# Optimization experiments

Measured on AMD Instinct MI355X. Metric: run time of the kernel, lower is better.

## Reference

```python
import jax, jax.numpy as jnp
import numpy as np

B, T, D, H = 8, 2048, 1024, 128  # batch, seq (== block_size), n_embd, head_size


def setup_inputs() -> dict:
    key = jax.random.key(0)
    kx, kq, kk, kv = jax.random.split(key, 4)
    s = D ** -0.5  # rough linear-init scale
    return {
        "x": jax.random.normal(kx, (B, T, D), dtype=jnp.float32),
        "Wq": jax.random.normal(kq, (D, H), dtype=jnp.float32) * s,
        "Wk": jax.random.normal(kk, (D, H), dtype=jnp.float32) * s,
        "Wv": jax.random.normal(kv, (D, H), dtype=jnp.float32) * s,
    }


def reference(x, Wq, Wk, Wv):
    # Linear projections (no bias)
    q = x @ Wq  # [B, T, H]
    k = x @ Wk  # [B, T, H]
    v = x @ Wv  # [B, T, H]
    scale = k.shape[-1] ** -0.5
    scores = jnp.einsum("bth,bsh->bts", q, k) * scale  # [B, T, T]
    # causal mask from tril buffer
    causal = jnp.tril(jnp.ones((T, T), dtype=bool))
    scores = jnp.where(causal, scores, jnp.finfo(scores.dtype).min)
    att = jax.nn.softmax(scores, axis=-1)
    out = jnp.einsum("bts,bsh->bth", att, v)  # [B, T, H]
    return out
```

## Files before the change

### kernel.cpp

```cpp
#include <hip/hip_runtime.h>
#include <hip/hip_bf16.h>
#include <stdint.h>

typedef float f32x4 __attribute__((ext_vector_type(4)));
typedef __bf16 bf16x8 __attribute__((ext_vector_type(8)));

#define T_SEQ 2048
#define D_EMB 1024
#define H_DIM 128
#define NBATCH 8
#define NTOK 16384

typedef __attribute__((address_space(3))) uint32_t lds_u32;
typedef const __attribute__((address_space(1))) uint32_t glb_u32;

#define DPPF(x, ctrl)                                                    \
  __int_as_float(__builtin_amdgcn_update_dpp(                            \
      0, __float_as_int(x), (ctrl), 0xF, 0xF, true))

#define PIPE_FENCE()                                       \
  do {                                                     \
    asm volatile("s_waitcnt vmcnt(0)" ::: "memory");       \
    __builtin_amdgcn_s_barrier();                          \
    __builtin_amdgcn_sched_barrier(0);                     \
  } while (0)


__global__ __launch_bounds__(256) void prep_w_kernel(
    const float* __restrict__ Wq, const float* __restrict__ Wk,
    const float* __restrict__ Wv, __hip_bfloat16* __restrict__ Wt) {
  __shared__ float T[128][133];
  const int mat = blockIdx.x >> 3;
  const int kc = blockIdx.x & 7;
  const float* W = (mat == 0) ? Wq : ((mat == 1) ? Wk : Wv);
  const int tid = threadIdx.x;
  const int k0 = kc * 128;
#pragma unroll 8
  for (int i = 0; i < 64; ++i) {
    const int e = i * 256 + tid;
    const int k = e >> 7, h = e & 127;
    T[k][h] = W[(size_t)(k0 + k) * H_DIM + h];
  }
  __syncthreads();
#pragma unroll 8
  for (int i = 0; i < 64; ++i) {
    const int e = i * 256 + tid;
    const int h = e >> 7, k = e & 127;
    Wt[((size_t)mat * 128 + h) * D_EMB + k0 + k] = __float2bfloat16(T[k][h]);
  }
}

__global__ __launch_bounds__(512) void proj_kernel(
    const float* __restrict__ x, const __hip_bfloat16* __restrict__ Wt,
    __hip_bfloat16* __restrict__ qb, __hip_bfloat16* __restrict__ kb,
    __hip_bfloat16* __restrict__ vt) {
  __shared__ __align__(16) float Af[2][64 * 64];
  __shared__ __align__(16) __hip_bfloat16 Bs[2][384 * 64];
  const int tid = threadIdx.x;
  const int wave = tid >> 6;
  const int lane = tid & 63;
  const int g = lane >> 4;
  const int lr = lane & 15;
  const int m0 = blockIdx.x * 64;
  const int wc = wave * 48;

  f32x4 acc[4][3];
#pragma unroll
  for (int m = 0; m < 4; ++m)
#pragma unroll
    for (int n = 0; n < 3; ++n) acc[m][n] = f32x4{0.f, 0.f, 0.f, 0.f};

  auto stageA = [&](int buf, int k0) {
#pragma unroll
    for (int i = 0; i < 2; ++i) {
      const int e = i * 512 + tid;
      const int row = e >> 4;
      const int un = e & 15;
      __builtin_amdgcn_global_load_lds(
          (glb_u32*)(uintptr_t)(x + (size_t)(m0 + row) * D_EMB + k0 +
                                ((un ^ (row & 15)) * 4)),
          (lds_u32*)(uintptr_t)(&Af[buf][e * 4]), 16, 0, 0);
    }
  };
  auto stageB = [&](int buf, int k0) {
#pragma unroll
    for (int i = 0; i < 6; ++i) {
      const int u = i * 512 + tid;
      const int row = u >> 3;
      const int chunk = u & 7;
      __builtin_amdgcn_global_load_lds(
          (glb_u32*)(uintptr_t)(Wt + (size_t)row * D_EMB + k0 +
                                ((chunk ^ (row & 7)) * 8)),
          (lds_u32*)(uintptr_t)(&Bs[buf][row * 64 + chunk * 8]), 16, 0, 0);
    }
  };
  auto compute = [&](int buf) {
#pragma unroll
    for (int kk = 0; kk < 2; ++kk) {
      bf16x8 a[4];
#pragma unroll
      for (int m = 0; m < 4; ++m) {
        const int row = m * 16 + lr;
        const int u0 = kk * 8 + g * 2;
        const f32x4 lo = *reinterpret_cast<const f32x4*>(
            &Af[buf][row * 64 + ((u0 ^ (row & 15)) * 4)]);
        const f32x4 hi = *reinterpret_cast<const f32x4*>(
            &Af[buf][row * 64 + (((u0 + 1) ^ (row & 15)) * 4)]);
        union { bf16x8 v; __hip_bfloat16 h[8]; } u;
        u.h[0] = __float2bfloat16(lo[0]);
        u.h[1] = __float2bfloat16(lo[1]);
        u.h[2] = __float2bfloat16(lo[2]);
        u.h[3] = __float2bfloat16(lo[3]);
        u.h[4] = __float2bfloat16(hi[0]);
        u.h[5] = __float2bfloat16(hi[1]);
        u.h[6] = __float2bfloat16(hi[2]);
        u.h[7] = __float2bfloat16(hi[3]);
        a[m] = u.v;
      }
#pragma unroll
      for (int n = 0; n < 3; ++n) {
        const int row = wc + n * 16 + lr;
        bf16x8 b = *reinterpret_cast<const bf16x8*>(
            &Bs[buf][row * 64 + (((kk * 4 + g) ^ (row & 7)) * 8)]);
#pragma unroll
        for (int m = 0; m < 4; ++m)
          acc[m][n] =
              __builtin_amdgcn_mfma_f32_16x16x32_bf16(a[m], b, acc[m][n], 0, 0, 0);
      }
    }
  };

  stageA(0, 0);
  stageB(0, 0);

  int cur = 0;
  for (int k = 0; k < 16; ++k) {
    PIPE_FENCE();
    if (k < 15) {
      stageA(cur ^ 1, (k + 1) * 64);
      stageB(cur ^ 1, (k + 1) * 64);
    }
    compute(cur);
    cur ^= 1;
  }

#pragma unroll
  for (int n = 0; n < 3; ++n) {
    const int ng = wc + n * 16 + lr;
    const int head = ng >> 7;
    const int h = ng & 127;
#pragma unroll
    for (int m = 0; m < 4; ++m) {
#pragma unroll
      for (int r = 0; r < 4; ++r) {
        const int row = m0 + m * 16 + g * 4 + r;
        const __hip_bfloat16 val = __float2bfloat16(acc[m][n][r]);
        if (head == 0) {
          qb[(size_t)row * H_DIM + h] = val;
        } else if (head == 1) {
          kb[(size_t)row * H_DIM + h] = val;
        } else {
          const int bi = row >> 11;
          const int t = row & (T_SEQ - 1);
          vt[((size_t)bi * H_DIM + h) * T_SEQ + t] = val;
        }
      }
    }
  }
}

__global__ __launch_bounds__(512) void attn_kernel(
    const __hip_bfloat16* __restrict__ qb, const __hip_bfloat16* __restrict__ kb,
    const __hip_bfloat16* __restrict__ vt, float* __restrict__ out,
    float* __restrict__ PA_O, float* __restrict__ PA_ml,
    float* __restrict__ PB_O, float* __restrict__ PB_ml) {
  __shared__ __align__(16) __hip_bfloat16 KV[2][16384];
  __shared__ __align__(16) __hip_bfloat16 Pl[8][16][40];
  __shared__ float Obuf[4][16][132];
  __shared__ float mbuf[8][16];
  __shared__ float lbuf[8][16];

  const int tid = threadIdx.x;
  const int wave = tid >> 6;
  const int lane = tid & 63;
  const int g = lane >> 4;
  const int lr = lane & 15;
  const int qt = wave >> 1;
  const int kp = wave & 1;
  const int idx = blockIdx.x;
  const int b = idx & 7;
  const int u = idx >> 3;

  const __hip_bfloat16* qB = qb + (size_t)b * T_SEQ * H_DIM;
  const __hip_bfloat16* kB = kb + (size_t)b * T_SEQ * H_DIM;
  const __hip_bfloat16* vB = vt + (size_t)b * H_DIM * T_SEQ;
  const float scale = 0.08838834764831845f;

  auto stage = [&](__hip_bfloat16* buf, int s0) {
#pragma unroll
    for (int i = 0; i < 2; ++i) {
      const int uu = tid + i * 512;
      const int row = uu >> 4, grp = uu & 15;
      __builtin_amdgcn_global_load_lds(
          (glb_u32*)(uintptr_t)(kB + (size_t)(s0 + row) * H_DIM +
                                ((grp ^ (row & 15)) * 8)),
          (lds_u32*)(uintptr_t)(buf + uu * 8), 16, 0, 0);
    }
#pragma unroll
    for (int i = 0; i < 2; ++i) {
      const int uu = tid + i * 512;
      const int h = uu >> 3, grp = uu & 7;
      __builtin_amdgcn_global_load_lds(
          (glb_u32*)(uintptr_t)(vB + (size_t)h * T_SEQ + s0 +
                                ((grp ^ (h & 7)) * 8)),
          (lds_u32*)(uintptr_t)(buf + 8192 + uu * 8), 16, 0, 0);
    }
  };

  auto process = [&](int tile, int rr0, int rr1, int mode) {
    const int qrow0 = tile * 64 + qt * 16;
    bf16x8 qf[4];
#pragma unroll
    for (int kt = 0; kt < 4; ++kt)
      qf[kt] = *reinterpret_cast<const bf16x8*>(
          qB + (size_t)(qrow0 + lr) * H_DIM + kt * 32 + g * 8);

    f32x4 oacc[8];
#pragma unroll
    for (int i = 0; i < 8; ++i) oacc[i] = f32x4{0.f, 0.f, 0.f, 0.f};
    float mrow[4] = {-1e30f, -1e30f, -1e30f, -1e30f};
    float lrow[4] = {0.f, 0.f, 0.f, 0.f};

    __hip_bfloat16* bufA = &KV[0][0];
    __hip_bfloat16* bufB = &KV[1][0];
    stage(bufA, rr0 * 64);

    for (int r = rr0; r <= rr1; ++r) {
      PIPE_FENCE();
      if (r < rr1) stage(bufB, (r + 1) * 64);
      const int s0 = r * 64;
      const bool active = (s0 + kp * 32) <= (qrow0 + 15);
      if (active) {
        f32x4 sacc[2];
        sacc[0] = f32x4{0.f, 0.f, 0.f, 0.f};
        sacc[1] = f32x4{0.f, 0.f, 0.f, 0.f};
#pragma unroll
        for (int nt = 0; nt < 2; ++nt) {
          const int kl = kp * 32 + nt * 16 + lr;
          const __hip_bfloat16* kr = bufA + kl * 128;
#pragma unroll
          for (int kt = 0; kt < 4; ++kt) {
            bf16x8 kf = *reinterpret_cast<const bf16x8*>(
                kr + (((kt * 4 + g) ^ (kl & 15)) * 8));
            sacc[nt] = __builtin_amdgcn_mfma_f32_16x16x32_bf16(qf[kt], kf,
                                                               sacc[nt], 0, 0, 0);
          }
        }
        bf16x8 vf[8];
#pragma unroll
        for (int ht = 0; ht < 8; ++ht) {
          const int h = ht * 16 + lr;
          vf[ht] = *reinterpret_cast<const bf16x8*>(
              bufA + 8192 + h * 64 + (((kp * 4 + g) ^ (h & 7)) * 8));
        }
        float sv[2][4];
#pragma unroll
        for (int nt = 0; nt < 2; ++nt)
#pragma unroll
          for (int rr = 0; rr < 4; ++rr) {
            const int key = s0 + kp * 32 + nt * 16 + lr;
            const int qr = qrow0 + g * 4 + rr;
            const float s = sacc[nt][rr] * scale;
            sv[nt][rr] = (key > qr) ? -1e30f : s;
          }
        float pm[4];
#pragma unroll
        for (int rr = 0; rr < 4; ++rr) pm[rr] = fmaxf(sv[0][rr], sv[1][rr]);
#pragma unroll
        for (int rr = 0; rr < 4; ++rr) {
          pm[rr] = fmaxf(pm[rr], DPPF(pm[rr], 0xB1));
          pm[rr] = fmaxf(pm[rr], DPPF(pm[rr], 0x4E));
          pm[rr] = fmaxf(pm[rr], DPPF(pm[rr], 0x141));
          pm[rr] = fmaxf(pm[rr], DPPF(pm[rr], 0x140));
        }
        bool ok = true;
#pragma unroll
        for (int rr = 0; rr < 4; ++rr) ok = ok && (pm[rr] <= mrow[rr] + 8.f);
        if (!__all((int)ok)) {
#pragma unroll
          for (int rr = 0; rr < 4; ++rr) {
            const float mnew = fmaxf(mrow[rr], pm[rr]);
            const float corr = __expf(mrow[rr] - mnew);
            mrow[rr] = mnew;
            lrow[rr] *= corr;
#pragma unroll
            for (int ht = 0; ht < 8; ++ht) oacc[ht][rr] *= corr;
          }
        }
        float rs[4];
#pragma unroll
        for (int rr = 0; rr < 4; ++rr) {
          const float p0 = __expf(sv[0][rr] - mrow[rr]);
          const float p1 = __expf(sv[1][rr] - mrow[rr]);
          Pl[wave][g * 4 + rr][lr] = __float2bfloat16(p0);
          Pl[wave][g * 4 + rr][16 + lr] = __float2bfloat16(p1);
          rs[rr] = p0 + p1;
        }
#pragma unroll
        for (int rr = 0; rr < 4; ++rr) {
          rs[rr] += DPPF(rs[rr], 0xB1);
          rs[rr] += DPPF(rs[rr], 0x4E);
          rs[rr] += DPPF(rs[rr], 0x141);
          rs[rr] += DPPF(rs[rr], 0x140);
        }
#pragma unroll
        for (int rr = 0; rr < 4; ++rr) lrow[rr] += rs[rr];
        bf16x8 pf = *reinterpret_cast<const bf16x8*>(&Pl[wave][lr][g * 8]);
#pragma unroll
        for (int ht = 0; ht < 8; ++ht)
          oacc[ht] = __builtin_amdgcn_mfma_f32_16x16x32_bf16(pf, vf[ht],
                                                             oacc[ht], 0, 0, 0);
      }
      __hip_bfloat16* t = bufA; bufA = bufB; bufB = t;
    }

    __syncthreads();
    if (kp == 1) {
#pragma unroll
      for (int ht = 0; ht < 8; ++ht)
#pragma unroll
        for (int rr = 0; rr < 4; ++rr)
          Obuf[qt][g * 4 + rr][ht * 16 + lr] = oacc[ht][rr];
      if (lr == 0) {
#pragma unroll
        for (int rr = 0; rr < 4; ++rr) {
          mbuf[wave][g * 4 + rr] = mrow[rr];
          lbuf[wave][g * 4 + rr] = lrow[rr];
        }
      }
    }
    __syncthreads();
    if (kp == 0) {
#pragma unroll
      for (int rr = 0; rr < 4; ++rr) {
        const float mB = mbuf[wave + 1][g * 4 + rr];
        const float lB = lbuf[wave + 1][g * 4 + rr];
        const float M = fmaxf(mrow[rr], mB);
        const float a = __expf(mrow[rr] - M);
        const float bt = __expf(mB - M);
        lrow[rr] = a * lrow[rr] + bt * lB;
        mrow[rr] = M;
#pragma unroll
        for (int ht = 0; ht < 8; ++ht)
          oacc[ht][rr] =
              a * oacc[ht][rr] + bt * Obuf[qt][g * 4 + rr][ht * 16 + lr];
      }
      if (mode == 0) {
#pragma unroll
        for (int ht = 0; ht < 8; ++ht)
#pragma unroll
          for (int rr = 0; rr < 4; ++rr) {
            const int qr = qrow0 + g * 4 + rr;
            out[((size_t)b * T_SEQ + qr) * H_DIM + ht * 16 + lr] =
                oacc[ht][rr] / lrow[rr];
          }
      } else {
        float* PO = (mode == 1) ? PA_O : PB_O;
        float* Pm = (mode == 1) ? PA_ml : PB_ml;
        const int slot = tile - 16;
#pragma unroll
        for (int rr = 0; rr < 4; ++rr) {
          const size_t pr = (size_t)(b * 16 + slot) * 64 + qt * 16 + g * 4 + rr;
#pragma unroll
          for (int ht = 0; ht < 8; ++ht)
            PO[pr * 128 + ht * 16 + lr] = oacc[ht][rr];
          if (lr == 0) {
            Pm[pr * 2 + 0] = mrow[rr];
            Pm[pr * 2 + 1] = lrow[rr];
          }
        }
      }
    }
    __syncthreads();
  };

  if (u < 16) {
    process(u, 0, u, 0);
    process(31 - u, 0, 15 - u, 1);
  } else {
    const int v = u - 16;
    process(31 - v, 16 - v, 31 - v, 2);
  }
}

__global__ __launch_bounds__(256) void combine_kernel(
    const float* __restrict__ PA_O, const float* __restrict__ PA_ml,
    const float* __restrict__ PB_O, const float* __restrict__ PB_ml,
    float* __restrict__ out) {
  const int b = blockIdx.x >> 4;
  const int s = blockIdx.x & 15;
  const int tid = threadIdx.x;
  const int row = tid >> 2;
  const int c0 = (tid & 3) * 32;
  const size_t pr = (size_t)(b * 16 + s) * 64 + row;
  const float mA = PA_ml[pr * 2], lA = PA_ml[pr * 2 + 1];
  const float mB = PB_ml[pr * 2], lB = PB_ml[pr * 2 + 1];
  const float M = fmaxf(mA, mB);
  const float a = __expf(mA - M), bb = __expf(mB - M);
  const float inv = 1.f / (a * lA + bb * lB);
  const float* oa = PA_O + pr * 128 + c0;
  const float* ob = PB_O + pr * 128 + c0;
  float* op = out + ((size_t)b * T_SEQ + (16 + s) * 64 + row) * H_DIM + c0;
#pragma unroll
  for (int i = 0; i < 32; i += 4) {
    const float4 x = *reinterpret_cast<const float4*>(oa + i);
    const float4 y = *reinterpret_cast<const float4*>(ob + i);
    float4 z;
    z.x = (a * x.x + bb * y.x) * inv;
    z.y = (a * x.y + bb * y.y) * inv;
    z.z = (a * x.z + bb * y.z) * inv;
    z.w = (a * x.w + bb * y.w) * inv;
    *reinterpret_cast<float4*>(op + i) = z;
  }
}

extern "C" void kernel_launch(void* const* d_in, const int* in_sizes, int n_in,
                              void* d_out, int out_size, void* d_ws, size_t ws_size,
                              hipStream_t stream) {
  const float* x = (const float*)d_in[0];
  const float* Wq = (const float*)d_in[1];
  const float* Wk = (const float*)d_in[2];
  const float* Wv = (const float*)d_in[3];
  float* out = (float*)d_out;

  __hip_bfloat16* Wt = (__hip_bfloat16*)d_ws;
  __hip_bfloat16* qbuf = Wt + (size_t)3 * 128 * 1024;
  __hip_bfloat16* kbuf = qbuf + (size_t)NTOK * H_DIM;
  __hip_bfloat16* vbuf = kbuf + (size_t)NTOK * H_DIM;
  float* fbase = (float*)(vbuf + (size_t)NBATCH * H_DIM * T_SEQ);
  float* PA_O = fbase;
  float* PA_ml = PA_O + (size_t)1048576;
  float* PB_O = PA_ml + 16384;
  float* PB_ml = PB_O + (size_t)1048576;

  hipLaunchKernelGGL(prep_w_kernel, dim3(24), dim3(256), 0, stream, Wq, Wk, Wv, Wt);
  hipLaunchKernelGGL(proj_kernel, dim3(256), dim3(512), 0, stream, x, Wt, qbuf,
                     kbuf, vbuf);
  hipLaunchKernelGGL(attn_kernel, dim3(256), dim3(512), 0, stream, qbuf, kbuf,
                     vbuf, out, PA_O, PA_ml, PB_O, PB_ml);
  hipLaunchKernelGGL(combine_kernel, dim3(128), dim3(256), 0, stream, PA_O,
                     PA_ml, PB_O, PB_ml, out);
}
```

Measured before the change: 70.64 us.

## Replace direct global-to-LDS loads with register-staged prefetch in proj and attention

Both the projection GEMM and the attention kernel drop the global_load_lds direct-to-LDS path. Next-tile data is now loaded into registers before compute and written to LDS afterwards, with a plain __syncthreads replacing the vmcnt(0)+barrier fence. In the projection kernel, x is converted to bf16 once at LDS-write time instead of in every compute read, which halves A-tile LDS space and bandwidth. The cost is extra VGPRs to hold the prefetched tiles and an added LDS write pass per iteration.

```diff
diff --git a/kernel.cpp b/kernel.cpp
--- a/kernel.cpp
+++ b/kernel.cpp
@@ -11,19 +11,9 @@
 #define NBATCH 8
 #define NTOK 16384
 
-typedef __attribute__((address_space(3))) uint32_t lds_u32;
-typedef const __attribute__((address_space(1))) uint32_t glb_u32;
-
 #define DPPF(x, ctrl)                                                    \
   __int_as_float(__builtin_amdgcn_update_dpp(                            \
       0, __float_as_int(x), (ctrl), 0xF, 0xF, true))
-
-#define PIPE_FENCE()                                       \
-  do {                                                     \
-    asm volatile("s_waitcnt vmcnt(0)" ::: "memory");       \
-    __builtin_amdgcn_s_barrier();                          \
-    __builtin_amdgcn_sched_barrier(0);                     \
-  } while (0)
 
 
 __global__ __launch_bounds__(256) void prep_w_kernel(
@@ -54,7 +44,7 @@
     const float* __restrict__ x, const __hip_bfloat16* __restrict__ Wt,
     __hip_bfloat16* __restrict__ qb, __hip_bfloat16* __restrict__ kb,
     __hip_bfloat16* __restrict__ vt) {
-  __shared__ __align__(16) float Af[2][64 * 64];
+  __shared__ __align__(16) __hip_bfloat16 As[2][64 * 64];
   __shared__ __align__(16) __hip_bfloat16 Bs[2][384 * 64];
   const int tid = threadIdx.x;
   const int wave = tid >> 6;
@@ -70,28 +60,44 @@
 #pragma unroll
     for (int n = 0; n < 3; ++n) acc[m][n] = f32x4{0.f, 0.f, 0.f, 0.f};
 
-  auto stageA = [&](int buf, int k0) {
-#pragma unroll
-    for (int i = 0; i < 2; ++i) {
-      const int e = i * 512 + tid;
-      const int row = e >> 4;
-      const int un = e & 15;
-      __builtin_amdgcn_global_load_lds(
-          (glb_u32*)(uintptr_t)(x + (size_t)(m0 + row) * D_EMB + k0 +
-                                ((un ^ (row & 15)) * 4)),
-          (lds_u32*)(uintptr_t)(&Af[buf][e * 4]), 16, 0, 0);
-    }
-  };
-  auto stageB = [&](int buf, int k0) {
+  const int arow = tid >> 3;
+  const int achunk = tid & 7;
+  const float* asrc = x + (size_t)(m0 + arow) * D_EMB + achunk * 8;
+
+  float4 fa0, fa1;
+  bf16x8 fb[6];
+
+  auto loads = [&](int k0) {
+    fa0 = *reinterpret_cast<const float4*>(asrc + k0);
+    fa1 = *reinterpret_cast<const float4*>(asrc + k0 + 4);
 #pragma unroll
     for (int i = 0; i < 6; ++i) {
       const int u = i * 512 + tid;
       const int row = u >> 3;
       const int chunk = u & 7;
-      __builtin_amdgcn_global_load_lds(
-          (glb_u32*)(uintptr_t)(Wt + (size_t)row * D_EMB + k0 +
-                                ((chunk ^ (row & 7)) * 8)),
-          (lds_u32*)(uintptr_t)(&Bs[buf][row * 64 + chunk * 8]), 16, 0, 0);
+      fb[i] = *reinterpret_cast<const bf16x8*>(
+          Wt + (size_t)row * D_EMB + k0 + chunk * 8);
+    }
+  };
+  auto writes = [&](int buf) {
+    union { bf16x8 v; __hip_bfloat16 h[8]; } u;
+    u.h[0] = __float2bfloat16(fa0.x);
+    u.h[1] = __float2bfloat16(fa0.y);
+    u.h[2] = __float2bfloat16(fa0.z);
+    u.h[3] = __float2bfloat16(fa0.w);
+    u.h[4] = __float2bfloat16(fa1.x);
+    u.h[5] = __float2bfloat16(fa1.y);
+    u.h[6] = __float2bfloat16(fa1.z);
+    u.h[7] = __float2bfloat16(fa1.w);
+    *reinterpret_cast<bf16x8*>(
+        &As[buf][arow * 64 + ((achunk ^ (arow & 7)) * 8)]) = u.v;
+#pragma unroll
+    for (int i = 0; i < 6; ++i) {
+      const int uu = i * 512 + tid;
+      const int row = uu >> 3;
+      const int chunk = uu & 7;
+      *reinterpret_cast<bf16x8*>(
+          &Bs[buf][row * 64 + ((chunk ^ (row & 7)) * 8)]) = fb[i];
     }
   };
   auto compute = [&](int buf) {
@@ -101,27 +107,14 @@
 #pragma unroll
       for (int m = 0; m < 4; ++m) {
         const int row = m * 16 + lr;
-        const int u0 = kk * 8 + g * 2;
-        const f32x4 lo = *reinterpret_cast<const f32x4*>(
-            &Af[buf][row * 64 + ((u0 ^ (row & 15)) * 4)]);
-        const f32x4 hi = *reinterpret_cast<const f32x4*>(
-            &Af[buf][row * 64 + (((u0 + 1) ^ (row & 15)) * 4)]);
-        union { bf16x8 v; __hip_bfloat16 h[8]; } u;
-        u.h[0] = __float2bfloat16(lo[0]);
-        u.h[1] = __float2bfloat16(lo[1]);
-        u.h[2] = __float2bfloat16(lo[2]);
-        u.h[3] = __float2bfloat16(lo[3]);
-        u.h[4] = __float2bfloat16(hi[0]);
-        u.h[5] = __float2bfloat16(hi[1]);
-        u.h[6] = __float2bfloat16(hi[2]);
-        u.h[7] = __float2bfloat16(hi[3]);
-        a[m] = u.v;
+        a[m] = *reinterpret_cast<const bf16x8*>(
+            &As[buf][row * 64 + (((kk * 4 + g) ^ (row & 7)) * 8)]);
       }
 #pragma unroll
       for (int n = 0; n < 3; ++n) {
-        const int row = wc + n * 16 + lr;
+        const int col = wc + n * 16 + lr;
         bf16x8 b = *reinterpret_cast<const bf16x8*>(
-            &Bs[buf][row * 64 + (((kk * 4 + g) ^ (row & 7)) * 8)]);
+            &Bs[buf][col * 64 + (((kk * 4 + g) ^ (col & 7)) * 8)]);
 #pragma unroll
         for (int m = 0; m < 4; ++m)
           acc[m][n] =
@@ -130,17 +123,16 @@
     }
   };
 
-  stageA(0, 0);
-  stageB(0, 0);
+  loads(0);
+  writes(0);
+  __syncthreads();
 
   int cur = 0;
   for (int k = 0; k < 16; ++k) {
-    PIPE_FENCE();
-    if (k < 15) {
-      stageA(cur ^ 1, (k + 1) * 64);
-      stageB(cur ^ 1, (k + 1) * 64);
-    }
+    if (k < 15) loads((k + 1) * 64);
     compute(cur);
+    if (k < 15) writes(cur ^ 1);
+    __syncthreads();
     cur ^= 1;
   }
 
@@ -196,24 +188,37 @@
   const __hip_bfloat16* vB = vt + (size_t)b * H_DIM * T_SEQ;
   const float scale = 0.08838834764831845f;
 
-  auto stage = [&](__hip_bfloat16* buf, int s0) {
+  bf16x8 kvreg[4];
+  auto loadKV = [&](int s0) {
 #pragma unroll
     for (int i = 0; i < 2; ++i) {
       const int uu = tid + i * 512;
       const int row = uu >> 4, grp = uu & 15;
-      __builtin_amdgcn_global_load_lds(
-          (glb_u32*)(uintptr_t)(kB + (size_t)(s0 + row) * H_DIM +
-                                ((grp ^ (row & 15)) * 8)),
-          (lds_u32*)(uintptr_t)(buf + uu * 8), 16, 0, 0);
+      kvreg[i] = *reinterpret_cast<const bf16x8*>(
+          kB + (size_t)(s0 + row) * H_DIM + grp * 8);
     }
 #pragma unroll
     for (int i = 0; i < 2; ++i) {
       const int uu = tid + i * 512;
       const int h = uu >> 3, grp = uu & 7;
-      __builtin_amdgcn_global_load_lds(
-          (glb_u32*)(uintptr_t)(vB + (size_t)h * T_SEQ + s0 +
-                                ((grp ^ (h & 7)) * 8)),
-          (lds_u32*)(uintptr_t)(buf + 8192 + uu * 8), 16, 0, 0);
+      kvreg[2 + i] = *reinterpret_cast<const bf16x8*>(
+          vB + (size_t)h * T_SEQ + s0 + grp * 8);
+    }
+  };
+  auto writeKV = [&](__hip_bfloat16* buf) {
+#pragma unroll
+    for (int i = 0; i < 2; ++i) {
+      const int uu = tid + i * 512;
+      const int row = uu >> 4, grp = uu & 15;
+      *reinterpret_cast<bf16x8*>(buf + row * 128 + ((grp ^ (row & 15)) * 8)) =
+          kvreg[i];
+    }
+#pragma unroll
+    for (int i = 0; i < 2; ++i) {
+      const int uu = tid + i * 512;
+      const int h = uu >> 3, grp = uu & 7;
+      *reinterpret_cast<bf16x8*>(buf + 8192 + h * 64 + ((grp ^ (h & 7)) * 8)) =
+          kvreg[2 + i];
     }
   };
 
@@ -233,11 +238,12 @@
 
     __hip_bfloat16* bufA = &KV[0][0];
     __hip_bfloat16* bufB = &KV[1][0];
-    stage(bufA, rr0 * 64);
+    loadKV(rr0 * 64);
+    writeKV(bufA);
+    __syncthreads();
 
     for (int r = rr0; r <= rr1; ++r) {
-      PIPE_FENCE();
-      if (r < rr1) stage(bufB, (r + 1) * 64);
+      if (r < rr1) loadKV((r + 1) * 64);
       const int s0 = r * 64;
       const bool active = (s0 + kp * 32) <= (qrow0 + 15);
       if (active) {
@@ -321,6 +327,8 @@
           oacc[ht] = __builtin_amdgcn_mfma_f32_16x16x32_bf16(pf, vf[ht],
                                                              oacc[ht], 0, 0, 0);
       }
+      if (r < rr1) writeKV(bufB);
+      __syncthreads();
       __hip_bfloat16* t = bufA; bufA = bufB; bufB = t;
     }
 
```

Measured after the change: 75.82 us. +7.3%, slower.

## Triple-buffer projection and attention loads; split projection columns across two blocks

Applied to the files above, without the earlier changes.

Moves both the projection and attention kernels from double to triple LDS buffering. Each iteration now waits on a partial vmcnt, so the prefetch for tile k+2 stays in flight while tile k is computed, instead of draining all loads before every barrier. The projection kernel is also split so each 256-thread block computes half of the 384 output columns, doubling the grid to 512 blocks. The costs are more LDS per block, which can lower occupancy in the attention kernel, and x tiles are now loaded twice, once by each column-half block.

```diff
diff --git a/kernel.cpp b/kernel.cpp
--- a/kernel.cpp
+++ b/kernel.cpp
@@ -18,11 +18,11 @@
   __int_as_float(__builtin_amdgcn_update_dpp(                            \
       0, __float_as_int(x), (ctrl), 0xF, 0xF, true))
 
-#define PIPE_FENCE()                                       \
-  do {                                                     \
-    asm volatile("s_waitcnt vmcnt(0)" ::: "memory");       \
-    __builtin_amdgcn_s_barrier();                          \
-    __builtin_amdgcn_sched_barrier(0);                     \
+#define WAIT_VM(n) asm volatile("s_waitcnt vmcnt(" #n ")" ::: "memory")
+#define BARRIER_PIN()                      \
+  do {                                     \
+    __builtin_amdgcn_s_barrier();          \
+    __builtin_amdgcn_sched_barrier(0);     \
   } while (0)
 
 
@@ -50,19 +50,21 @@
   }
 }
 
-__global__ __launch_bounds__(512) void proj_kernel(
+__global__ __launch_bounds__(256) void proj_kernel(
     const float* __restrict__ x, const __hip_bfloat16* __restrict__ Wt,
     __hip_bfloat16* __restrict__ qb, __hip_bfloat16* __restrict__ kb,
     __hip_bfloat16* __restrict__ vt) {
-  __shared__ __align__(16) float Af[2][64 * 64];
-  __shared__ __align__(16) __hip_bfloat16 Bs[2][384 * 64];
+  __shared__ __align__(16) float Af[3][64 * 64];
+  __shared__ __align__(16) __hip_bfloat16 Bs[3][192 * 64];
   const int tid = threadIdx.x;
   const int wave = tid >> 6;
   const int lane = tid & 63;
   const int g = lane >> 4;
   const int lr = lane & 15;
-  const int m0 = blockIdx.x * 64;
-  const int wc = wave * 48;
+  const int hh = blockIdx.x & 1;
+  const int m0 = (blockIdx.x >> 1) * 64;
+  const int wcl = wave * 48;
+  const __hip_bfloat16* WtH = Wt + (size_t)hh * 192 * D_EMB;
 
   f32x4 acc[4][3];
 #pragma unroll
@@ -70,10 +72,10 @@
 #pragma unroll
     for (int n = 0; n < 3; ++n) acc[m][n] = f32x4{0.f, 0.f, 0.f, 0.f};
 
-  auto stageA = [&](int buf, int k0) {
-#pragma unroll
-    for (int i = 0; i < 2; ++i) {
-      const int e = i * 512 + tid;
+  auto stage = [&](int buf, int k0) {
+#pragma unroll
+    for (int i = 0; i < 4; ++i) {
+      const int e = i * 256 + tid;
       const int row = e >> 4;
       const int un = e & 15;
       __builtin_amdgcn_global_load_lds(
@@ -81,15 +83,13 @@
                                 ((un ^ (row & 15)) * 4)),
           (lds_u32*)(uintptr_t)(&Af[buf][e * 4]), 16, 0, 0);
     }
-  };
-  auto stageB = [&](int buf, int k0) {
 #pragma unroll
     for (int i = 0; i < 6; ++i) {
-      const int u = i * 512 + tid;
+      const int u = i * 256 + tid;
       const int row = u >> 3;
       const int chunk = u & 7;
       __builtin_amdgcn_global_load_lds(
-          (glb_u32*)(uintptr_t)(Wt + (size_t)row * D_EMB + k0 +
+          (glb_u32*)(uintptr_t)(WtH + (size_t)row * D_EMB + k0 +
                                 ((chunk ^ (row & 7)) * 8)),
           (lds_u32*)(uintptr_t)(&Bs[buf][row * 64 + chunk * 8]), 16, 0, 0);
     }
@@ -119,9 +119,9 @@
       }
 #pragma unroll
       for (int n = 0; n < 3; ++n) {
-        const int row = wc + n * 16 + lr;
+        const int col = wcl + n * 16 + lr;
         bf16x8 b = *reinterpret_cast<const bf16x8*>(
-            &Bs[buf][row * 64 + (((kk * 4 + g) ^ (row & 7)) * 8)]);
+            &Bs[buf][col * 64 + (((kk * 4 + g) ^ (col & 7)) * 8)]);
 #pragma unroll
         for (int m = 0; m < 4; ++m)
           acc[m][n] =
@@ -130,23 +130,19 @@
     }
   };
 
-  stageA(0, 0);
-  stageB(0, 0);
-
-  int cur = 0;
+  stage(0, 0);
+  stage(1, 64);
+
   for (int k = 0; k < 16; ++k) {
-    PIPE_FENCE();
-    if (k < 15) {
-      stageA(cur ^ 1, (k + 1) * 64);
-      stageB(cur ^ 1, (k + 1) * 64);
-    }
-    compute(cur);
-    cur ^= 1;
+    if (k < 15) { WAIT_VM(10); } else { WAIT_VM(0); }
+    BARRIER_PIN();
+    if (k + 2 < 16) stage((k + 2) % 3, (k + 2) * 64);
+    compute(k % 3);
   }
 
 #pragma unroll
   for (int n = 0; n < 3; ++n) {
-    const int ng = wc + n * 16 + lr;
+    const int ng = hh * 192 + wcl + n * 16 + lr;
     const int head = ng >> 7;
     const int h = ng & 127;
 #pragma unroll
@@ -174,7 +170,7 @@
     const __hip_bfloat16* __restrict__ vt, float* __restrict__ out,
     float* __restrict__ PA_O, float* __restrict__ PA_ml,
     float* __restrict__ PB_O, float* __restrict__ PB_ml) {
-  __shared__ __align__(16) __hip_bfloat16 KV[2][16384];
+  __shared__ __align__(16) __hip_bfloat16 KV[3][16384];
   __shared__ __align__(16) __hip_bfloat16 Pl[8][16][40];
   __shared__ float Obuf[4][16][132];
   __shared__ float mbuf[8][16];
@@ -196,7 +192,8 @@
   const __hip_bfloat16* vB = vt + (size_t)b * H_DIM * T_SEQ;
   const float scale = 0.08838834764831845f;
 
-  auto stage = [&](__hip_bfloat16* buf, int s0) {
+  auto stage = [&](int buf, int s0) {
+    __hip_bfloat16* dst = &KV[buf][0];
 #pragma unroll
     for (int i = 0; i < 2; ++i) {
       const int uu = tid + i * 512;
@@ -204,7 +201,7 @@
       __builtin_amdgcn_global_load_lds(
           (glb_u32*)(uintptr_t)(kB + (size_t)(s0 + row) * H_DIM +
                                 ((grp ^ (row & 15)) * 8)),
-          (lds_u32*)(uintptr_t)(buf + uu * 8), 16, 0, 0);
+          (lds_u32*)(uintptr_t)(dst + uu * 8), 16, 0, 0);
     }
 #pragma unroll
     for (int i = 0; i < 2; ++i) {
@@ -213,7 +210,7 @@
       __builtin_amdgcn_global_load_lds(
           (glb_u32*)(uintptr_t)(vB + (size_t)h * T_SEQ + s0 +
                                 ((grp ^ (h & 7)) * 8)),
-          (lds_u32*)(uintptr_t)(buf + 8192 + uu * 8), 16, 0, 0);
+          (lds_u32*)(uintptr_t)(dst + 8192 + uu * 8), 16, 0, 0);
     }
   };
 
@@ -231,13 +228,14 @@
     float mrow[4] = {-1e30f, -1e30f, -1e30f, -1e30f};
     float lrow[4] = {0.f, 0.f, 0.f, 0.f};
 
-    __hip_bfloat16* bufA = &KV[0][0];
-    __hip_bfloat16* bufB = &KV[1][0];
-    stage(bufA, rr0 * 64);
+    stage(rr0 % 3, rr0 * 64);
+    if (rr0 + 1 <= rr1) stage((rr0 + 1) % 3, (rr0 + 1) * 64);
 
     for (int r = rr0; r <= rr1; ++r) {
-      PIPE_FENCE();
-      if (r < rr1) stage(bufB, (r + 1) * 64);
+      if (r < rr1) { WAIT_VM(4); } else { WAIT_VM(0); }
+      BARRIER_PIN();
+      if (r + 2 <= rr1) stage((r + 2) % 3, (r + 2) * 64);
+      const __hip_bfloat16* bufA = &KV[r % 3][0];
       const int s0 = r * 64;
       const bool active = (s0 + kp * 32) <= (qrow0 + 15);
       if (active) {
@@ -321,7 +319,6 @@
           oacc[ht] = __builtin_amdgcn_mfma_f32_16x16x32_bf16(pf, vf[ht],
                                                              oacc[ht], 0, 0, 0);
       }
-      __hip_bfloat16* t = bufA; bufA = bufB; bufB = t;
     }
 
     __syncthreads();
@@ -444,7 +441,7 @@
   float* PB_ml = PB_O + (size_t)1048576;
 
   hipLaunchKernelGGL(prep_w_kernel, dim3(24), dim3(256), 0, stream, Wq, Wk, Wv, Wt);
-  hipLaunchKernelGGL(proj_kernel, dim3(256), dim3(512), 0, stream, x, Wt, qbuf,
+  hipLaunchKernelGGL(proj_kernel, dim3(512), dim3(256), 0, stream, x, Wt, qbuf,
                      kbuf, vbuf);
   hipLaunchKernelGGL(attn_kernel, dim3(256), dim3(512), 0, stream, qbuf, kbuf,
                      vbuf, out, PA_O, PA_ml, PB_O, PB_ml);
```

New measurement: 85.87 us. 1.22x slower.
